# Kernel optimization log

Measured on AMD Instinct MI355X. Metric: run time of the kernel, lower is better.

Reference implementation:

```python
import jax, jax.numpy as jnp
import numpy as np

N_BINS = 15
N = 1_000_000
C = 128


def setup_inputs() -> dict:
    key = jax.random.key(0)
    k1, k2 = jax.random.split(key)
    logits = jax.random.normal(k1, (N, C), dtype=jnp.float32)
    labels = jax.random.randint(k2, (N,), 0, C, dtype=jnp.int64)
    return {"logits": logits, "labels": labels}


def reference(logits, labels):
    # softmax -> per-sample confidence (max prob) and prediction (argmax)
    probs = jax.nn.softmax(logits, axis=1)
    confidences = jnp.max(probs, axis=1)          # [N]
    predictions = jnp.argmax(probs, axis=1)       # [N]
    accuracies = (predictions == labels).astype(jnp.float32)  # [N]

    # bin_lowers = linspace(0,1,n_bins+1)[:-1]; sample falls in bin i if
    # conf >= lower_i and conf < lower_{i+1} (last bin closed at 1.0).
    bin_lowers = jnp.linspace(0.0, 1.0, N_BINS + 1)[:-1]
    bin_idx = jnp.searchsorted(bin_lowers, confidences, side="right") - 1
    bin_idx = jnp.clip(bin_idx, 0, N_BINS - 1)

    correct = jax.ops.segment_sum(accuracies, bin_idx, num_segments=N_BINS)
    total = jax.ops.segment_sum(jnp.ones_like(accuracies), bin_idx, num_segments=N_BINS)
    # column 0: correct count in bin; column 1: incorrect count in bin
    bin_stats = jnp.stack([correct, total - correct], axis=1)  # [N_BINS, 2]
    return bin_stats
```

## Files before the change

### kernel.cpp

```cpp
#include <hip/hip_runtime.h>

#define N_BINS 15
#define NCLASS 128

__global__ void zero_out_kernel(float* __restrict__ out) {
    int i = threadIdx.x;
    if (i < 2 * N_BINS) out[i] = 0.0f;
}

__device__ __forceinline__ int dpp_xor1_i(int x) {
    return __builtin_amdgcn_mov_dpp(x, 0xB1, 0xF, 0xF, true);
}
__device__ __forceinline__ int dpp_xor2_i(int x) {
    return __builtin_amdgcn_mov_dpp(x, 0x4E, 0xF, 0xF, true);
}
__device__ __forceinline__ float dpp_xor1_f(float x) {
    return __int_as_float(dpp_xor1_i(__float_as_int(x)));
}
__device__ __forceinline__ float dpp_xor2_f(float x) {
    return __int_as_float(dpp_xor2_i(__float_as_int(x)));
}

__global__ __launch_bounds__(256) void conf_hist_kernel(
        const float* __restrict__ logits,
        const int* __restrict__ labels,
        float* __restrict__ out,
        int n) {
    __shared__ int hist[2 * N_BINS];
    if (threadIdx.x < 2 * N_BINS) hist[threadIdx.x] = 0;
    __syncthreads();

    const int lane = threadIdx.x & 63;
    const int quad = lane >> 2;
    const int t = lane & 3;
    const int wavesPerBlock = blockDim.x >> 6;
    const int wave = blockIdx.x * wavesPerBlock + (threadIdx.x >> 6);
    const int numWaves = gridDim.x * wavesPerBlock;

    for (int base = wave * 16; base < n; base += numWaves * 16) {
        const int s = base + quad;
        if (s < n) {
            const float* row = logits + (size_t)s * NCLASS + t * 4;
            float4 c[8];
            #pragma unroll
            for (int j = 0; j < 8; ++j)
                c[j] = *(const float4*)(row + j * 16);

            float m[8]; int mi[8];
            #pragma unroll
            for (int j = 0; j < 8; ++j) {
                float mm = c[j].x; int ii = 0;
                if (c[j].y > mm) { mm = c[j].y; ii = 1; }
                if (c[j].z > mm) { mm = c[j].z; ii = 2; }
                if (c[j].w > mm) { mm = c[j].w; ii = 3; }
                m[j] = mm; mi[j] = j * 16 + t * 4 + ii;
            }
            #pragma unroll
            for (int stp = 1; stp < 8; stp <<= 1) {
                #pragma unroll
                for (int j = 0; j < 8; j += 2 * stp) {
                    if (m[j + stp] > m[j]) { m[j] = m[j + stp]; mi[j] = mi[j + stp]; }
                }
            }
            float bm = m[0]; int bi = mi[0];

            {
                float om = dpp_xor1_f(bm); int oi = dpp_xor1_i(bi);
                if (om > bm || (om == bm && oi < bi)) { bm = om; bi = oi; }
            }
            {
                float om = dpp_xor2_f(bm); int oi = dpp_xor2_i(bi);
                if (om > bm || (om == bm && oi < bi)) { bm = om; bi = oi; }
            }

            float s4[8];
            #pragma unroll
            for (int j = 0; j < 8; ++j)
                s4[j] = (__expf(c[j].x - bm) + __expf(c[j].y - bm))
                      + (__expf(c[j].z - bm) + __expf(c[j].w - bm));
            float e = ((s4[0] + s4[1]) + (s4[2] + s4[3]))
                    + ((s4[4] + s4[5]) + (s4[6] + s4[7]));
            e += dpp_xor1_f(e);
            e += dpp_xor2_f(e);

            if (t == 0) {
                float conf = 1.0f / e;
                int bin = (int)(conf * (float)N_BINS);
                bin = bin > (N_BINS - 1) ? (N_BINS - 1) : (bin < 0 ? 0 : bin);
                int col = (bi == labels[s]) ? 0 : 1;
                atomicAdd(&hist[bin * 2 + col], 1);
            }
        }
    }

    __syncthreads();
    if (threadIdx.x < 2 * N_BINS) {
        int c = hist[threadIdx.x];
        if (c != 0) atomicAdd(&out[threadIdx.x], (float)c);
    }
}

extern "C" void kernel_launch(void* const* d_in, const int* in_sizes, int n_in,
                              void* d_out, int out_size, void* d_ws, size_t ws_size,
                              hipStream_t stream) {
    const float* logits = (const float*)d_in[0];
    const int*   labels = (const int*)d_in[1];
    float* out = (float*)d_out;
    const int n = in_sizes[1];

    zero_out_kernel<<<1, 64, 0, stream>>>(out);

    const int block = 256;
    const int grid = 2048;
    conf_hist_kernel<<<grid, block, 0, stream>>>(logits, labels, out, n);
}
```

Before: 652.2 us.

## Software-pipeline logits loads with nontemporal prefetch of next row tile

```diff
diff --git a/kernel.cpp b/kernel.cpp
--- a/kernel.cpp
+++ b/kernel.cpp
@@ -2,6 +2,8 @@
 
 #define N_BINS 15
 #define NCLASS 128
+
+typedef float fx4 __attribute__((ext_vector_type(4)));
 
 __global__ void zero_out_kernel(float* __restrict__ out) {
     int i = threadIdx.x;
@@ -21,7 +23,7 @@
     return __int_as_float(dpp_xor2_i(__float_as_int(x)));
 }
 
-__global__ __launch_bounds__(256) void conf_hist_kernel(
+__global__ __launch_bounds__(256, 4) void conf_hist_kernel(
         const float* __restrict__ logits,
         const int* __restrict__ labels,
         float* __restrict__ out,
@@ -36,23 +38,48 @@
     const int wavesPerBlock = blockDim.x >> 6;
     const int wave = blockIdx.x * wavesPerBlock + (threadIdx.x >> 6);
     const int numWaves = gridDim.x * wavesPerBlock;
+    const int stride = numWaves * 16;
 
-    for (int base = wave * 16; base < n; base += numWaves * 16) {
+    int base = wave * 16;
+    fx4 cA[8];
+    int labA = 0;
+    {
         const int s = base + quad;
-        if (s < n) {
+        if (base < n && s < n) {
             const float* row = logits + (size_t)s * NCLASS + t * 4;
-            float4 c[8];
             #pragma unroll
             for (int j = 0; j < 8; ++j)
-                c[j] = *(const float4*)(row + j * 16);
+                cA[j] = __builtin_nontemporal_load((const fx4*)(row + j * 16));
+            labA = labels[s];
+        }
+    }
 
+    for (; base < n; base += stride) {
+        const int s = base + quad;
+
+        const int nbase = base + stride;
+        const int ns = nbase + quad;
+        fx4 cB[8];
+        int labB = 0;
+        if (nbase < n && ns < n) {
+            const float* row = logits + (size_t)ns * NCLASS + t * 4;
+            #pragma unroll
+            for (int j = 0; j < 8; ++j)
+                cB[j] = __builtin_nontemporal_load((const fx4*)(row + j * 16));
+            labB = labels[ns];
+        } else {
+            #pragma unroll
+            for (int j = 0; j < 8; ++j) cB[j] = (fx4)(0.0f);
+        }
+
+        if (s < n) {
             float m[8]; int mi[8];
             #pragma unroll
             for (int j = 0; j < 8; ++j) {
-                float mm = c[j].x; int ii = 0;
-                if (c[j].y > mm) { mm = c[j].y; ii = 1; }
-                if (c[j].z > mm) { mm = c[j].z; ii = 2; }
-                if (c[j].w > mm) { mm = c[j].w; ii = 3; }
+                float mm = cA[j][0]; int ii = 0;
+                if (cA[j][1] > mm) { mm = cA[j][1]; ii = 1; }
+                if (cA[j][2] > mm) { mm = cA[j][2]; ii = 2; }
+                if (cA[j][3] > mm) { mm = cA[j][3]; ii = 3; }
                 m[j] = mm; mi[j] = j * 16 + t * 4 + ii;
             }
             #pragma unroll
@@ -76,8 +103,8 @@
             float s4[8];
             #pragma unroll
             for (int j = 0; j < 8; ++j)
-                s4[j] = (__expf(c[j].x - bm) + __expf(c[j].y - bm))
-                      + (__expf(c[j].z - bm) + __expf(c[j].w - bm));
+                s4[j] = (__expf(cA[j][0] - bm) + __expf(cA[j][1] - bm))
+                      + (__expf(cA[j][2] - bm) + __expf(cA[j][3] - bm));
             float e = ((s4[0] + s4[1]) + (s4[2] + s4[3]))
                     + ((s4[4] + s4[5]) + (s4[6] + s4[7]));
             e += dpp_xor1_f(e);
@@ -87,10 +114,14 @@
                 float conf = 1.0f / e;
                 int bin = (int)(conf * (float)N_BINS);
                 bin = bin > (N_BINS - 1) ? (N_BINS - 1) : (bin < 0 ? 0 : bin);
-                int col = (bi == labels[s]) ? 0 : 1;
+                int col = (bi == labA) ? 0 : 1;
                 atomicAdd(&hist[bin * 2 + col], 1);
             }
         }
+
+        #pragma unroll
+        for (int j = 0; j < 8; ++j) cA[j] = cB[j];
+        labA = labB;
     }
 
     __syncthreads();
```

Result: faster. 629.2 us (-3.5%).

## Coalesce row loads across half-waves and double-buffer next tile in registers

Applied to the files above, without the earlier changes.

```diff
diff --git a/kernel.cpp b/kernel.cpp
--- a/kernel.cpp
+++ b/kernel.cpp
@@ -2,6 +2,8 @@
 
 #define N_BINS 15
 #define NCLASS 128
+
+typedef float fx4 __attribute__((ext_vector_type(4)));
 
 __global__ void zero_out_kernel(float* __restrict__ out) {
     int i = threadIdx.x;
@@ -14,14 +16,16 @@
 __device__ __forceinline__ int dpp_xor2_i(int x) {
     return __builtin_amdgcn_mov_dpp(x, 0x4E, 0xF, 0xF, true);
 }
-__device__ __forceinline__ float dpp_xor1_f(float x) {
-    return __int_as_float(dpp_xor1_i(__float_as_int(x)));
-}
-__device__ __forceinline__ float dpp_xor2_f(float x) {
-    return __int_as_float(dpp_xor2_i(__float_as_int(x)));
-}
+__device__ __forceinline__ int swz_xor4_i(int x)  { return __builtin_amdgcn_ds_swizzle(x, 0x101F); }
+__device__ __forceinline__ int swz_xor8_i(int x)  { return __builtin_amdgcn_ds_swizzle(x, 0x201F); }
+__device__ __forceinline__ int swz_xor16_i(int x) { return __builtin_amdgcn_ds_swizzle(x, 0x401F); }
+__device__ __forceinline__ float dpp_xor1_f(float x)  { return __int_as_float(dpp_xor1_i(__float_as_int(x))); }
+__device__ __forceinline__ float dpp_xor2_f(float x)  { return __int_as_float(dpp_xor2_i(__float_as_int(x))); }
+__device__ __forceinline__ float swz_xor4_f(float x)  { return __int_as_float(swz_xor4_i(__float_as_int(x))); }
+__device__ __forceinline__ float swz_xor8_f(float x)  { return __int_as_float(swz_xor8_i(__float_as_int(x))); }
+__device__ __forceinline__ float swz_xor16_f(float x) { return __int_as_float(swz_xor16_i(__float_as_int(x))); }
 
-__global__ __launch_bounds__(256) void conf_hist_kernel(
+__global__ __launch_bounds__(256, 4) void conf_hist_kernel(
         const float* __restrict__ logits,
         const int* __restrict__ labels,
         float* __restrict__ out,
@@ -31,66 +35,80 @@
     __syncthreads();
 
     const int lane = threadIdx.x & 63;
-    const int quad = lane >> 2;
-    const int t = lane & 3;
+    const int half = lane >> 5;
+    const int c32 = lane & 31;
     const int wavesPerBlock = blockDim.x >> 6;
     const int wave = blockIdx.x * wavesPerBlock + (threadIdx.x >> 6);
     const int numWaves = gridDim.x * wavesPerBlock;
+    const int stride = numWaves * 16;
 
-    for (int base = wave * 16; base < n; base += numWaves * 16) {
-        const int s = base + quad;
-        if (s < n) {
-            const float* row = logits + (size_t)s * NCLASS + t * 4;
-            float4 c[8];
+    const float* lanep = logits + lane * 4;
+
+    int base = wave * 16;
+    fx4 cA[8];
+    int labA = 0;
+    if (base < n) {
+        const float* pb = lanep + (size_t)base * NCLASS;
+        #pragma unroll
+        for (int p = 0; p < 8; ++p) cA[p] = *(const fx4*)(pb + p * 256);
+        labA = labels[base + (c32 & 15)];
+    }
+
+    for (; base < n; base += stride) {
+        const int nbase = base + stride;
+        fx4 cB[8];
+        int labB = 0;
+        if (nbase < n) {
+            const float* pb = lanep + (size_t)nbase * NCLASS;
             #pragma unroll
-            for (int j = 0; j < 8; ++j)
-                c[j] = *(const float4*)(row + j * 16);
+            for (int p = 0; p < 8; ++p) cB[p] = *(const fx4*)(pb + p * 256);
+            labB = labels[nbase + (c32 & 15)];
+        } else {
+            #pragma unroll
+            for (int p = 0; p < 8; ++p) cB[p] = (fx4)(0.0f);
+        }
 
-            float m[8]; int mi[8];
-            #pragma unroll
-            for (int j = 0; j < 8; ++j) {
-                float mm = c[j].x; int ii = 0;
-                if (c[j].y > mm) { mm = c[j].y; ii = 1; }
-                if (c[j].z > mm) { mm = c[j].z; ii = 2; }
-                if (c[j].w > mm) { mm = c[j].w; ii = 3; }
-                m[j] = mm; mi[j] = j * 16 + t * 4 + ii;
-            }
-            #pragma unroll
-            for (int stp = 1; stp < 8; stp <<= 1) {
-                #pragma unroll
-                for (int j = 0; j < 8; j += 2 * stp) {
-                    if (m[j + stp] > m[j]) { m[j] = m[j + stp]; mi[j] = mi[j + stp]; }
-                }
-            }
-            float bm = m[0]; int bi = mi[0];
+        #pragma unroll
+        for (int p = 0; p < 8; ++p) {
+            const fx4 v = cA[p];
 
-            {
-                float om = dpp_xor1_f(bm); int oi = dpp_xor1_i(bi);
-                if (om > bm || (om == bm && oi < bi)) { bm = om; bi = oi; }
-            }
-            {
-                float om = dpp_xor2_f(bm); int oi = dpp_xor2_i(bi);
-                if (om > bm || (om == bm && oi < bi)) { bm = om; bi = oi; }
-            }
+            float mm = v[0]; int ii = 0;
+            if (v[1] > mm) { mm = v[1]; ii = 1; }
+            if (v[2] > mm) { mm = v[2]; ii = 2; }
+            if (v[3] > mm) { mm = v[3]; ii = 3; }
+            float bm = mm; int bi = (c32 << 2) + ii;
 
-            float s4[8];
-            #pragma unroll
-            for (int j = 0; j < 8; ++j)
-                s4[j] = (__expf(c[j].x - bm) + __expf(c[j].y - bm))
-                      + (__expf(c[j].z - bm) + __expf(c[j].w - bm));
-            float e = ((s4[0] + s4[1]) + (s4[2] + s4[3]))
-                    + ((s4[4] + s4[5]) + (s4[6] + s4[7]));
+            { float om = dpp_xor1_f(bm);  int oi = dpp_xor1_i(bi);
+              if (om > bm || (om == bm && oi < bi)) { bm = om; bi = oi; } }
+            { float om = dpp_xor2_f(bm);  int oi = dpp_xor2_i(bi);
+              if (om > bm || (om == bm && oi < bi)) { bm = om; bi = oi; } }
+            { float om = swz_xor4_f(bm);  int oi = swz_xor4_i(bi);
+              if (om > bm || (om == bm && oi < bi)) { bm = om; bi = oi; } }
+            { float om = swz_xor8_f(bm);  int oi = swz_xor8_i(bi);
+              if (om > bm || (om == bm && oi < bi)) { bm = om; bi = oi; } }
+            { float om = swz_xor16_f(bm); int oi = swz_xor16_i(bi);
+              if (om > bm || (om == bm && oi < bi)) { bm = om; bi = oi; } }
+
+            float e = (__expf(v[0] - bm) + __expf(v[1] - bm))
+                    + (__expf(v[2] - bm) + __expf(v[3] - bm));
             e += dpp_xor1_f(e);
             e += dpp_xor2_f(e);
+            e += swz_xor4_f(e);
+            e += swz_xor8_f(e);
+            e += swz_xor16_f(e);
 
-            if (t == 0) {
+            if (c32 == 2 * p + half) {
                 float conf = 1.0f / e;
                 int bin = (int)(conf * (float)N_BINS);
                 bin = bin > (N_BINS - 1) ? (N_BINS - 1) : (bin < 0 ? 0 : bin);
-                int col = (bi == labels[s]) ? 0 : 1;
+                int col = (bi == labA) ? 0 : 1;
                 atomicAdd(&hist[bin * 2 + col], 1);
             }
         }
+
+        #pragma unroll
+        for (int p = 0; p < 8; ++p) cA[p] = cB[p];
+        labA = labB;
     }
 
     __syncthreads();
@@ -111,6 +129,6 @@
     zero_out_kernel<<<1, 64, 0, stream>>>(out);
 
     const int block = 256;
-    const int grid = 2048;
+    const int grid = 1024;
     conf_hist_kernel<<<grid, block, 0, stream>>>(logits, labels, out, n);
 }
```

Measured after the change: 685.7 us. 5.1% more time.
